# Kernel tuning notes

Measured on AMD Instinct MI355X. Metric: run time of the kernel, lower is better.

The kernel has to match this reference:

```python
import jax, jax.numpy as jnp
import numpy as np
import math

EPS = 1e-8
DIM, HEADS, K = 256, 8, 16
HD = DIM // HEADS
B, N, PDIM = 4, 4096, 3


def _layernorm(x, w, b, eps=1e-5):
    m = jnp.mean(x, axis=-1, keepdims=True)
    v = jnp.mean((x - m) ** 2, axis=-1, keepdims=True)
    return (x - m) * jax.lax.rsqrt(v + eps) * w + b


def setup_inputs() -> dict:
    key = jax.random.key(0)
    ks = jax.random.split(key, 16)
    s = 0.02
    d = {
        'x': jax.random.normal(ks[0], (B, N, DIM), jnp.float32),
        'positions': jax.random.uniform(ks[1], (B, N, PDIM), jnp.float32) * 0.5,  # inside unit ball
        'c': jnp.ones((1,), jnp.float32),
        'time_emb': jax.random.normal(ks[2], (B, DIM), jnp.float32),
        'Wq': jax.random.normal(ks[3], (DIM, DIM), jnp.float32) * s,
        'bq': jnp.zeros((DIM,), jnp.float32),
        'Wk': jax.random.normal(ks[4], (DIM, DIM), jnp.float32) * s,
        'bk': jnp.zeros((DIM,), jnp.float32),
        'Wv': jax.random.normal(ks[5], (DIM, DIM), jnp.float32) * s,
        'bv': jnp.zeros((DIM,), jnp.float32),
        'Wo': jax.random.normal(ks[6], (DIM, DIM), jnp.float32) * s,
        'bo': jnp.zeros((DIM,), jnp.float32),
        'W1': jax.random.normal(ks[7], (DIM, 4 * DIM), jnp.float32) * s,
        'b1': jnp.zeros((4 * DIM,), jnp.float32),
        'W2': jax.random.normal(ks[8], (4 * DIM, DIM), jnp.float32) * s,
        'b2': jnp.zeros((DIM,), jnp.float32),
        'ln1_w': jnp.ones((DIM,), jnp.float32),
        'ln1_b': jnp.zeros((DIM,), jnp.float32),
        'ln2_w': jnp.ones((DIM,), jnp.float32),
        'ln2_b': jnp.zeros((DIM,), jnp.float32),
        'log_tau': jnp.zeros((), jnp.float32),
    }
    return d


def _poincare_dist_matrix(pos, c):
    # pos: [B,N,P], c: scalar > 0. Returns [B,N,N] with d[b,i,j] = dist(pos[b,j], pos[b,i])
    sq = jnp.sum(pos ** 2, axis=-1)                      # [B,N]
    diff2 = (sq[:, :, None] + sq[:, None, :]
             - 2.0 * jnp.einsum('bip,bjp->bij', pos, pos))
    diff2 = jnp.maximum(diff2, 0.0)
    num = 2.0 * c * diff2
    den = (1.0 - c * sq[:, :, None]) * (1.0 - c * sq[:, None, :])
    arg = jnp.maximum(1.0 + num / (den + EPS), 1.0)
    return jnp.arccosh(arg) / jnp.sqrt(c)


def reference(x, positions, c, time_emb, Wq, bq, Wk, bk, Wv, bv, Wo, bo,
              W1, b1, W2, b2, ln1_w, ln1_b, ln2_w, ln2_b, log_tau):
    c_s = jnp.squeeze(c)
    x_res = x
    h = _layernorm(x, ln1_w, ln1_b) + time_emb[:, None, :]

    q = (h @ Wq + bq).reshape(B, N, HEADS, HD).transpose(0, 2, 1, 3)  # [B,H,N,hd]
    k = (h @ Wk + bk).reshape(B, N, HEADS, HD).transpose(0, 2, 1, 3)
    v = (h @ Wv + bv).reshape(B, N, HEADS, HD).transpose(0, 2, 1, 3)

    # pairwise hyperbolic distances + kNN (no_grad in original)
    dist = jax.lax.stop_gradient(_poincare_dist_matrix(positions, c_s))  # [B,N,N]
    neg_vals, idx = jax.lax.top_k(-dist, K)          # smallest-K distances
    attn_dists = -neg_vals                            # [B,N,K]

    # gather neighbor keys/values: out[b,h,n,j,d] = k[b,h,idx[b,n,j],d]
    idx_flat = idx.reshape(B, 1, N * K, 1)            # broadcast over heads, hd
    k_g = jnp.take_along_axis(k, idx_flat, axis=2).reshape(B, HEADS, N, K, HD)
    v_g = jnp.take_along_axis(v, idx_flat, axis=2).reshape(B, HEADS, N, K, HD)

    feat = jnp.einsum('bhnd,bhnkd->bhnk', q, k_g) / math.sqrt(HD)
    tau = jnp.exp(log_tau) + EPS
    scores = feat - attn_dists[:, None, :, :] / tau
    probs = jax.nn.softmax(scores, axis=-1)
    attn = jnp.einsum('bhnk,bhnkd->bhnd', probs, v_g)
    attn = attn.transpose(0, 2, 1, 3).reshape(B, N, DIM)

    x2 = x_res + attn @ Wo + bo
    ff = jax.nn.gelu(_layernorm(x2, ln2_w, ln2_b) @ W1 + b1, approximate=False) @ W2 + b2
    return x2 + ff
```

## Files before the change

kernel.cpp:

```cpp
#include <hip/hip_runtime.h>
#include <math.h>

namespace {

constexpr int kBatch = 4;
constexpr int kN = 4096;
constexpr int kDim = 256;
constexpr int kHeads = 8;
constexpr int kK = 16;
constexpr float kEps = 1e-8f;

using u16 = unsigned short;
typedef __attribute__((ext_vector_type(8))) short short8;
typedef __attribute__((ext_vector_type(8))) u16 u16x8;
typedef __attribute__((ext_vector_type(4))) float f32x4;

__device__ __forceinline__ float b2f(u16 u) {
  union { unsigned int i; float f; } x; x.i = ((unsigned int)u) << 16; return x.f;
}
__device__ __forceinline__ u16 f2b(float f) {
  union { float f; unsigned int i; } x; x.f = f;
  unsigned int r = x.i + 0x7fffu + ((x.i >> 16) & 1u);
  return (u16)(r >> 16);
}
__device__ __forceinline__ float gelu_exact(float x) {
  return 0.5f * x * (1.0f + erff(x * 0.70710678118654752f));
}
__device__ __forceinline__ void load_lds16(const u16* g, u16* l) {
  __builtin_amdgcn_global_load_lds(
      (const __attribute__((address_space(1))) unsigned int*)g,
      (__attribute__((address_space(3))) unsigned int*)l, 16, 0, 0);
}

template<bool ADD_TEMB>
__global__ __launch_bounds__(256) void ln_kernel(
    const float* __restrict__ x, const float* __restrict__ w,
    const float* __restrict__ bb, const float* __restrict__ temb,
    u16* __restrict__ out) {
  int gt = blockIdx.x * 256 + threadIdx.x;
  int row = gt >> 6;
  int lane = threadIdx.x & 63;
  const float4* xr = (const float4*)(x + (size_t)row * kDim);
  float4 v = xr[lane];
  float s = v.x + v.y + v.z + v.w;
  #pragma unroll
  for (int off = 32; off; off >>= 1) s += __shfl_xor(s, off);
  float mean = s * (1.0f / kDim);
  float dx = v.x - mean, dy = v.y - mean, dz = v.z - mean, dw = v.w - mean;
  float ss = dx * dx + dy * dy + dz * dz + dw * dw;
  #pragma unroll
  for (int off = 32; off; off >>= 1) ss += __shfl_xor(ss, off);
  float rstd = rsqrtf(ss * (1.0f / kDim) + 1e-5f);
  float4 wv = ((const float4*)w)[lane];
  float4 bv = ((const float4*)bb)[lane];
  float ox = dx * rstd * wv.x + bv.x;
  float oy = dy * rstd * wv.y + bv.y;
  float oz = dz * rstd * wv.z + bv.z;
  float ow = dw * rstd * wv.w + bv.w;
  if (ADD_TEMB) {
    int bi = row >> 12;
    float4 t = ((const float4*)(temb + (size_t)bi * kDim))[lane];
    ox += t.x; oy += t.y; oz += t.z; ow += t.w;
  }
  ushort4 ob;
  ob.x = f2b(ox); ob.y = f2b(oy); ob.z = f2b(oz); ob.w = f2b(ow);
  ((ushort4*)(out + (size_t)row * kDim))[lane] = ob;
}

__global__ __launch_bounds__(256) void wtrans_kernel(
    const float* __restrict__ Wq, const float* __restrict__ Wk,
    const float* __restrict__ Wv, const float* __restrict__ Wo,
    const float* __restrict__ W1, const float* __restrict__ W2,
    u16* __restrict__ Tq, u16* __restrict__ Tk,
    u16* __restrict__ Tv, u16* __restrict__ To,
    u16* __restrict__ T1, u16* __restrict__ T2) {
  __shared__ float t[32][33];
  int bx = blockIdx.x;
  int seg = bx >> 8, e = bx & 255;
  const float* W; u16* T; int Kin, Nin, kt, nt;
  if (seg == 0) {
    int which = e >> 6, tl = e & 63;
    W = which == 0 ? Wq : which == 1 ? Wk : which == 2 ? Wv : Wo;
    T = which == 0 ? Tq : which == 1 ? Tk : which == 2 ? Tv : To;
    Kin = 256; Nin = 256; kt = tl >> 3; nt = tl & 7;
  } else if (seg == 1) {
    W = W1; T = T1; Kin = 256; Nin = 1024; kt = e >> 5; nt = e & 31;
  } else {
    W = W2; T = T2; Kin = 1024; Nin = 256; kt = e >> 3; nt = e & 7;
  }
  int tx = threadIdx.x & 31, ty = threadIdx.x >> 5;
  #pragma unroll
  for (int rr = 0; rr < 4; ++rr) {
    int r = rr * 8 + ty;
    t[r][tx] = W[(size_t)(kt * 32 + r) * Nin + nt * 32 + tx];
  }
  __syncthreads();
  #pragma unroll
  for (int rr = 0; rr < 4; ++rr) {
    int r = rr * 8 + ty;
    T[(size_t)(nt * 32 + r) * Kin + kt * 32 + tx] = f2b(t[tx][r]);
  }
}

template<int EPI, int BN>
__device__ __forceinline__ void gemm_body(
    const u16* __restrict__ A, const u16* __restrict__ Bt,
    const float* __restrict__ bias, const float* __restrict__ R,
    float* __restrict__ Cf, u16* __restrict__ Cbf,
    int N, int K, int bx, int by) {
  constexpr int NI = BN / 32;
  __shared__ u16 Al[128 * 32];
  __shared__ u16 Bl[BN * 32];
  int tid = threadIdx.x;
  int wv = tid >> 6, ln = tid & 63;
  int wr = wv >> 1, wc = wv & 1;
  int lhi = ln >> 4, llo = ln & 15;
  int bm = bx * 128, bn = by * BN;

  f32x4 zero = {0.f, 0.f, 0.f, 0.f};
  f32x4 acc[4][NI];
  #pragma unroll
  for (int mi = 0; mi < 4; ++mi)
    #pragma unroll
    for (int ni = 0; ni < NI; ++ni) acc[mi][ni] = zero;

  for (int k0 = 0; k0 < K; k0 += 32) {
    if (k0) __syncthreads();
    #pragma unroll
    for (int i = 0; i < 2; ++i) {
      int f = i * 256 + tid;
      int r = f >> 2, kp = f & 3;
      load_lds16(A + (size_t)(bm + r) * K + k0 + kp * 8,
                 &Al[(i * 256 + wv * 64) * 8]);
    }
    #pragma unroll
    for (int i = 0; i < BN / 64; ++i) {
      int f = i * 256 + tid;
      int r = f >> 2, kp = f & 3;
      load_lds16(Bt + (size_t)(bn + r) * K + k0 + kp * 8,
                 &Bl[(i * 256 + wv * 64) * 8]);
    }
    __syncthreads();
    short8 af[4], bf[NI];
    #pragma unroll
    for (int mi = 0; mi < 4; ++mi)
      af[mi] = *(const short8*)&Al[(wr * 64 + mi * 16 + llo) * 32 + lhi * 8];
    #pragma unroll
    for (int ni = 0; ni < NI; ++ni)
      bf[ni] = *(const short8*)&Bl[(wc * (BN / 2) + ni * 16 + llo) * 32 + lhi * 8];
    #pragma unroll
    for (int mi = 0; mi < 4; ++mi)
      #pragma unroll
      for (int ni = 0; ni < NI; ++ni)
        acc[mi][ni] = __builtin_amdgcn_mfma_f32_16x16x32_bf16(
            af[mi], bf[ni], acc[mi][ni], 0, 0, 0);
  }

  #pragma unroll
  for (int mi = 0; mi < 4; ++mi) {
    #pragma unroll
    for (int r = 0; r < 4; ++r) {
      int row = bm + wr * 64 + mi * 16 + lhi * 4 + r;
      #pragma unroll
      for (int ni = 0; ni < NI; ++ni) {
        int col = bn + wc * (BN / 2) + ni * 16 + llo;
        float val = acc[mi][ni][r] + bias[col];
        if (EPI == 1) {
          val += R[(size_t)row * N + col];
          Cf[(size_t)row * N + col] = val;
        } else {
          if (EPI == 2) val = gelu_exact(val);
          Cbf[(size_t)row * N + col] = f2b(val);
        }
      }
    }
  }
}

template<int EPI, int BN>
__global__ __launch_bounds__(256) void gemm_kernel(
    const u16* __restrict__ A, const u16* __restrict__ Bt,
    const float* __restrict__ bias, const float* __restrict__ R,
    float* __restrict__ Cf, u16* __restrict__ Cbf, int N, int K) {
  gemm_body<EPI, BN>(A, Bt, bias, R, Cf, Cbf, N, K, blockIdx.x, blockIdx.y);
}

__global__ __launch_bounds__(256) void qkv_kernel(
    const u16* __restrict__ A,
    const u16* __restrict__ Bq, const u16* __restrict__ Bk, const u16* __restrict__ Bv,
    const float* __restrict__ bq, const float* __restrict__ bk, const float* __restrict__ bv,
    u16* __restrict__ q, u16* __restrict__ k, u16* __restrict__ v) {
  int sel = blockIdx.y >> 1;
  const u16* Bt = sel == 0 ? Bq : sel == 1 ? Bk : Bv;
  const float* bias = sel == 0 ? bq : sel == 1 ? bk : bv;
  u16* C = sel == 0 ? q : sel == 1 ? k : v;
  gemm_body<0, 128>(A, Bt, bias, nullptr, nullptr, C, 256, 256,
                    blockIdx.x, blockIdx.y & 1);
}

__global__ __launch_bounds__(1024, 4) void topk_kernel(
    const float* __restrict__ pos, const float* __restrict__ cptr,
    int* __restrict__ idx_out, float* __restrict__ dist_out) {
  __shared__ float4 ps[kN];
  int tid = threadIdx.x;
  int wave = tid >> 6, ln = tid & 63;
  int row = blockIdx.x * 16 + wave;
  int b = row >> 12;
  float c = cptr[0];
  const float* pb = pos + (size_t)b * kN * 3;
  for (int j = tid; j < kN; j += 1024) {
    float x = pb[j * 3 + 0], y = pb[j * 3 + 1], z = pb[j * 3 + 2];
    ps[j] = make_float4(x, y, z, c * (x * x + y * y + z * z));
  }
  __syncthreads();

  int i = row & (kN - 1);
  float4 pi = ps[i];
  float wi = pi.w, oi = 1.0f - wi;
  float sx = 2.0f * c * pi.x, sy = 2.0f * c * pi.y, sz = 2.0f * c * pi.z;

  auto numden = [&](int j, float& num, float& den) {
    float4 pj = ps[j];
    float tt = wi + pj.w;
    tt = fmaf(-sx, pj.x, tt);
    tt = fmaf(-sy, pj.y, tt);
    tt = fmaf(-sz, pj.z, tt);
    num = fmaxf(tt, 0.0f);
    den = fmaf(-oi, pj.w, oi);
  };
  auto packkey = [&](float num, float den, int j) -> unsigned {
    float r = num * __builtin_amdgcn_rcpf(den);
    union { float f; unsigned u; } cv; cv.f = r;
    return (cv.u & 0xFFFFF000u) | (unsigned)j;
  };
  auto inflate = [&](unsigned T) -> float {
    union { unsigned u; float f; } tv; tv.u = T & 0xFFFFF000u;
    return fmaf(tv.f, 0.001f, tv.f);
  };

  float n0, d0;
  numden(ln, n0, d0);
  unsigned lpk = packkey(n0, d0, ln);
  #pragma unroll
  for (int kk = 2; kk <= 64; kk <<= 1) {
    #pragma unroll
    for (int jj = kk >> 1; jj >= 1; jj >>= 1) {
      unsigned ov = (unsigned)__shfl_xor((int)lpk, jj);
      bool keepMin = (((ln & kk) == 0) == ((ln & jj) == 0));
      bool less = ov < lpk;
      if (keepMin ? less : !less) lpk = ov;
    }
  }
  float Tf = inflate((unsigned)__builtin_amdgcn_readlane((int)lpk, 15));

  auto processGroup = [&](float num, float den, int base) {
    unsigned long long m = __ballot(num < Tf * den);
    if (m) {
      unsigned cpk = packkey(num, den, base + ln);
      do {
        int src = __ffsll(m) - 1;
        m &= m - 1;
        unsigned npk = (unsigned)__builtin_amdgcn_readlane((int)cpk, src);
        unsigned pv = (unsigned)__builtin_amdgcn_update_dpp(
            0, (int)lpk, 0x111 , 0xF, 0xF, false);
        bool gt = lpk > npk;
        bool take = gt && ((ln == 0) || (pv <= npk));
        lpk = take ? npk : (gt ? pv : lpk);
      } while (m);
      Tf = inflate((unsigned)__builtin_amdgcn_readlane((int)lpk, 15));
    }
  };

  int t = 1;
  for (; t + 3 < 64; t += 4) {
    float a0, b0, a1, b1, a2, b2, a3, b3;
    numden(ln + (t + 0) * 64, a0, b0);
    numden(ln + (t + 1) * 64, a1, b1);
    numden(ln + (t + 2) * 64, a2, b2);
    numden(ln + (t + 3) * 64, a3, b3);
    processGroup(a0, b0, (t + 0) * 64);
    processGroup(a1, b1, (t + 1) * 64);
    processGroup(a2, b2, (t + 2) * 64);
    processGroup(a3, b3, (t + 3) * 64);
  }
  for (; t < 64; ++t) {
    float a0, b0;
    numden(ln + t * 64, a0, b0);
    processGroup(a0, b0, t * 64);
  }

  if (ln < kK) {
    int j = (int)(lpk & 0xFFFu);
    float4 pj = ps[j];
    float tt = wi + pj.w;
    tt = fmaf(-sx, pj.x, tt);
    tt = fmaf(-sy, pj.y, tt);
    tt = fmaf(-sz, pj.z, tt);
    float num = 2.0f * fmaxf(tt, 0.0f);
    float den = fmaf(-oi, pj.w, oi) + kEps;
    float arg = fmaxf(1.0f + num / den, 1.0f);
    float rs = 1.0f / sqrtf(c);
    idx_out[(size_t)row * kK + ln] = j;
    dist_out[(size_t)row * kK + ln] = acoshf(arg) * rs;
  }
}

__global__ __launch_bounds__(256) void attn_kernel(
    const u16* __restrict__ q, const u16* __restrict__ k,
    const u16* __restrict__ v, const int* __restrict__ nidx,
    const float* __restrict__ ndist, const float* __restrict__ log_tau,
    u16* __restrict__ out) {
  int t = blockIdx.x * 256 + threadIdx.x;
  int h = t & (kHeads - 1);
  int row = t >> 3;
  int b = row >> 12;
  float rtau = 1.0f / (expf(log_tau[0]) + kEps);
  const u16x8* qr = (const u16x8*)(q + (size_t)row * kDim + h * 32);
  float qf[32];
  #pragma unroll
  for (int cch = 0; cch < 4; ++cch) {
    u16x8 u = qr[cch];
    #pragma unroll
    for (int e = 0; e < 8; ++e) qf[cch * 8 + e] = b2f(u[e]);
  }

  int njs[kK];
  float sc[kK];
  const int* ir = nidx + (size_t)row * kK;
  const float* dr = ndist + (size_t)row * kK;
  float smax = -1e30f;
  #pragma unroll
  for (int j = 0; j < kK; ++j) {
    int nj = ir[j];
    njs[j] = nj;
    const u16x8* kr = (const u16x8*)(k + ((size_t)b * kN + nj) * kDim + h * 32);
    float dot = 0.0f;
    #pragma unroll
    for (int cch = 0; cch < 4; ++cch) {
      u16x8 u = kr[cch];
      #pragma unroll
      for (int e = 0; e < 8; ++e) dot = fmaf(qf[cch * 8 + e], b2f(u[e]), dot);
    }
    float s = dot * 0.17677669529663687f - dr[j] * rtau;
    sc[j] = s;
    smax = fmaxf(smax, s);
  }
  float sum = 0.0f;
  #pragma unroll
  for (int j = 0; j < kK; ++j) { sc[j] = expf(sc[j] - smax); sum += sc[j]; }
  float rsum = 1.0f / sum;
  float o[32];
  #pragma unroll
  for (int d = 0; d < 32; ++d) o[d] = 0.0f;
  #pragma unroll
  for (int j = 0; j < kK; ++j) {
    float p = sc[j] * rsum;
    const u16x8* vr = (const u16x8*)(v + ((size_t)b * kN + njs[j]) * kDim + h * 32);
    #pragma unroll
    for (int cch = 0; cch < 4; ++cch) {
      u16x8 u = vr[cch];
      #pragma unroll
      for (int e = 0; e < 8; ++e) o[cch * 8 + e] = fmaf(p, b2f(u[e]), o[cch * 8 + e]);
    }
  }
  u16x8* orow = (u16x8*)(out + (size_t)row * kDim + h * 32);
  #pragma unroll
  for (int cch = 0; cch < 4; ++cch) {
    u16x8 po;
    #pragma unroll
    for (int e = 0; e < 8; ++e) po[e] = f2b(o[cch * 8 + e]);
    orow[cch] = po;
  }
}

}

extern "C" void kernel_launch(void* const* d_in, const int* in_sizes, int n_in,
                              void* d_out, int out_size, void* d_ws, size_t ws_size,
                              hipStream_t stream) {
  const float* x    = (const float*)d_in[0];
  const float* pos  = (const float*)d_in[1];
  const float* c    = (const float*)d_in[2];
  const float* temb = (const float*)d_in[3];
  const float* Wq   = (const float*)d_in[4];
  const float* bq   = (const float*)d_in[5];
  const float* Wk   = (const float*)d_in[6];
  const float* bk   = (const float*)d_in[7];
  const float* Wv   = (const float*)d_in[8];
  const float* bv   = (const float*)d_in[9];
  const float* Wo   = (const float*)d_in[10];
  const float* bo   = (const float*)d_in[11];
  const float* W1   = (const float*)d_in[12];
  const float* b1   = (const float*)d_in[13];
  const float* W2   = (const float*)d_in[14];
  const float* b2   = (const float*)d_in[15];
  const float* ln1w = (const float*)d_in[16];
  const float* ln1b = (const float*)d_in[17];
  const float* ln2w = (const float*)d_in[18];
  const float* ln2b = (const float*)d_in[19];
  const float* ltau = (const float*)d_in[20];

  const size_t MB = 1ull << 20;
  char* w = (char*)d_ws;
  u16*   h_bf  = (u16*)(w + 0 * MB);
  u16*   qb    = (u16*)(w + 8 * MB);
  u16*   kb    = (u16*)(w + 16 * MB);
  u16*   vb    = (u16*)(w + 24 * MB);
  u16*   attnb = (u16*)(w + 32 * MB);
  float* x2    = (float*)(w + 40 * MB);
  u16*   g_bf  = (u16*)(w + 56 * MB);
  u16*   wq_t  = (u16*)(w + 88 * MB);
  u16*   wk_t  = wq_t + 65536;
  u16*   wv_t  = wq_t + 2 * 65536;
  u16*   wo_t  = wq_t + 3 * 65536;
  u16*   w1_t  = (u16*)(w + 89 * MB);
  u16*   w2_t  = (u16*)(w + 89 * MB + 512 * 1024);
  int*   kidx  = (int*)(w + 90 * MB);
  float* kdst  = (float*)(w + 91 * MB);
  u16*   tln   = h_bf;

  hipLaunchKernelGGL(wtrans_kernel, dim3(768), dim3(256), 0, stream,
                     Wq, Wk, Wv, Wo, W1, W2, wq_t, wk_t, wv_t, wo_t, w1_t, w2_t);
  hipLaunchKernelGGL((ln_kernel<true>), dim3(4096), dim3(256), 0, stream,
                     x, ln1w, ln1b, temb, h_bf);
  hipLaunchKernelGGL(topk_kernel, dim3(1024), dim3(1024), 0, stream,
                     pos, c, kidx, kdst);
  hipLaunchKernelGGL(qkv_kernel, dim3(128, 6), dim3(256), 0, stream,
                     h_bf, wq_t, wk_t, wv_t, bq, bk, bv, qb, kb, vb);
  hipLaunchKernelGGL(attn_kernel, dim3(512), dim3(256), 0, stream,
                     qb, kb, vb, kidx, kdst, ltau, attnb);
  hipLaunchKernelGGL((gemm_kernel<1, 64>), dim3(128, 4), dim3(256), 0, stream,
                     attnb, wo_t, bo, x, x2, (u16*)nullptr, 256, 256);
  hipLaunchKernelGGL((ln_kernel<false>), dim3(4096), dim3(256), 0, stream,
                     x2, ln2w, ln2b, nullptr, tln);
  hipLaunchKernelGGL((gemm_kernel<2, 128>), dim3(128, 8), dim3(256), 0, stream,
                     tln, w1_t, b1, nullptr, (float*)nullptr, g_bf, 1024, 256);
  hipLaunchKernelGGL((gemm_kernel<1, 64>), dim3(128, 4), dim3(256), 0, stream,
                     g_bf, w2_t, b2, x2, (float*)d_out, (u16*)nullptr, 256, 1024);
}
```

Measured before the change: 179.5 us.

## Restructure GEMMs to stage whole B panels in swizzled LDS and stream A from registers

All GEMM kernels (QKV, output projection, FFN1, FFN2) are rewritten so that a 64-column B panel is staged into LDS in large K chunks with an XOR swizzle against bank conflicts. A operands are read straight from global memory into registers instead of through LDS, and there are far fewer barriers per K step. The grids now use BN=64 tiles, which doubles the block count for QKV and FFN1. The intent is to cut synchronization and LDS traffic. In exchange, the non-coalesced direct global A loads may go uncached and the larger LDS footprint may lower occupancy.

```diff
diff --git a/kernel.cpp b/kernel.cpp
--- a/kernel.cpp
+++ b/kernel.cpp
@@ -102,58 +102,61 @@
   }
 }
 
-template<int EPI, int BN>
-__device__ __forceinline__ void gemm_body(
+template<int EPI, int KTOT, int KCHUNK>
+__global__ __launch_bounds__(256) void gemm2_kernel(
     const u16* __restrict__ A, const u16* __restrict__ Bt,
     const float* __restrict__ bias, const float* __restrict__ R,
-    float* __restrict__ Cf, u16* __restrict__ Cbf,
-    int N, int K, int bx, int by) {
-  constexpr int NI = BN / 32;
-  __shared__ u16 Al[128 * 32];
-  __shared__ u16 Bl[BN * 32];
+    float* __restrict__ Cf, u16* __restrict__ Cbf, int N) {
+  __shared__ u16 Bl[64 * KCHUNK];
+  constexpr int OCT = KCHUNK / 8;
   int tid = threadIdx.x;
   int wv = tid >> 6, ln = tid & 63;
   int wr = wv >> 1, wc = wv & 1;
   int lhi = ln >> 4, llo = ln & 15;
-  int bm = bx * 128, bn = by * BN;
+  int bm = blockIdx.x * 128, bn = blockIdx.y * 64;
 
   f32x4 zero = {0.f, 0.f, 0.f, 0.f};
-  f32x4 acc[4][NI];
+  f32x4 acc[4][2];
   #pragma unroll
   for (int mi = 0; mi < 4; ++mi)
     #pragma unroll
-    for (int ni = 0; ni < NI; ++ni) acc[mi][ni] = zero;
-
-  for (int k0 = 0; k0 < K; k0 += 32) {
-    if (k0) __syncthreads();
-    #pragma unroll
-    for (int i = 0; i < 2; ++i) {
+    for (int ni = 0; ni < 2; ++ni) acc[mi][ni] = zero;
+
+  const u16* Arow[4];
+  #pragma unroll
+  for (int mi = 0; mi < 4; ++mi)
+    Arow[mi] = A + (size_t)(bm + wr * 64 + mi * 16 + llo) * KTOT + lhi * 8;
+
+  for (int kc = 0; kc < KTOT; kc += KCHUNK) {
+    if (kc) __syncthreads();
+    constexpr int NL = 64 * KCHUNK / (8 * 256);
+    #pragma unroll
+    for (int i = 0; i < NL; ++i) {
       int f = i * 256 + tid;
-      int r = f >> 2, kp = f & 3;
-      load_lds16(A + (size_t)(bm + r) * K + k0 + kp * 8,
-                 &Al[(i * 256 + wv * 64) * 8]);
-    }
-    #pragma unroll
-    for (int i = 0; i < BN / 64; ++i) {
-      int f = i * 256 + tid;
-      int r = f >> 2, kp = f & 3;
-      load_lds16(Bt + (size_t)(bn + r) * K + k0 + kp * 8,
+      int r = f / OCT, o = f % OCT;
+      load_lds16(Bt + (size_t)(bn + r) * KTOT + kc + ((o ^ (r & 7)) << 3),
                  &Bl[(i * 256 + wv * 64) * 8]);
     }
     __syncthreads();
-    short8 af[4], bf[NI];
-    #pragma unroll
-    for (int mi = 0; mi < 4; ++mi)
-      af[mi] = *(const short8*)&Al[(wr * 64 + mi * 16 + llo) * 32 + lhi * 8];
-    #pragma unroll
-    for (int ni = 0; ni < NI; ++ni)
-      bf[ni] = *(const short8*)&Bl[(wc * (BN / 2) + ni * 16 + llo) * 32 + lhi * 8];
-    #pragma unroll
-    for (int mi = 0; mi < 4; ++mi)
-      #pragma unroll
-      for (int ni = 0; ni < NI; ++ni)
-        acc[mi][ni] = __builtin_amdgcn_mfma_f32_16x16x32_bf16(
-            af[mi], bf[ni], acc[mi][ni], 0, 0, 0);
+    #pragma unroll
+    for (int k0 = 0; k0 < KCHUNK; k0 += 32) {
+      short8 af[4], bf[2];
+      #pragma unroll
+      for (int mi = 0; mi < 4; ++mi)
+        af[mi] = *(const short8*)(Arow[mi] + kc + k0);
+      #pragma unroll
+      for (int ni = 0; ni < 2; ++ni) {
+        int brow = wc * 32 + ni * 16 + llo;
+        int oct = ((k0 >> 3) + lhi) ^ (llo & 7);
+        bf[ni] = *(const short8*)&Bl[brow * KCHUNK + oct * 8];
+      }
+      #pragma unroll
+      for (int mi = 0; mi < 4; ++mi)
+        #pragma unroll
+        for (int ni = 0; ni < 2; ++ni)
+          acc[mi][ni] = __builtin_amdgcn_mfma_f32_16x16x32_bf16(
+              af[mi], bf[ni], acc[mi][ni], 0, 0, 0);
+    }
   }
 
   #pragma unroll
@@ -162,8 +165,8 @@
     for (int r = 0; r < 4; ++r) {
       int row = bm + wr * 64 + mi * 16 + lhi * 4 + r;
       #pragma unroll
-      for (int ni = 0; ni < NI; ++ni) {
-        int col = bn + wc * (BN / 2) + ni * 16 + llo;
+      for (int ni = 0; ni < 2; ++ni) {
+        int col = bn + wc * 32 + ni * 16 + llo;
         float val = acc[mi][ni][r] + bias[col];
         if (EPI == 1) {
           val += R[(size_t)row * N + col];
@@ -177,25 +180,72 @@
   }
 }
 
-template<int EPI, int BN>
-__global__ __launch_bounds__(256) void gemm_kernel(
-    const u16* __restrict__ A, const u16* __restrict__ Bt,
-    const float* __restrict__ bias, const float* __restrict__ R,
-    float* __restrict__ Cf, u16* __restrict__ Cbf, int N, int K) {
-  gemm_body<EPI, BN>(A, Bt, bias, R, Cf, Cbf, N, K, blockIdx.x, blockIdx.y);
-}
-
-__global__ __launch_bounds__(256) void qkv_kernel(
+__global__ __launch_bounds__(256) void qkv2_kernel(
     const u16* __restrict__ A,
     const u16* __restrict__ Bq, const u16* __restrict__ Bk, const u16* __restrict__ Bv,
     const float* __restrict__ bq, const float* __restrict__ bk, const float* __restrict__ bv,
     u16* __restrict__ q, u16* __restrict__ k, u16* __restrict__ v) {
-  int sel = blockIdx.y >> 1;
+  __shared__ u16 Bl[64 * 256];
+  int sel = blockIdx.y >> 2, by = blockIdx.y & 3;
   const u16* Bt = sel == 0 ? Bq : sel == 1 ? Bk : Bv;
   const float* bias = sel == 0 ? bq : sel == 1 ? bk : bv;
   u16* C = sel == 0 ? q : sel == 1 ? k : v;
-  gemm_body<0, 128>(A, Bt, bias, nullptr, nullptr, C, 256, 256,
-                    blockIdx.x, blockIdx.y & 1);
+
+  int tid = threadIdx.x;
+  int wv = tid >> 6, ln = tid & 63;
+  int wr = wv >> 1, wc = wv & 1;
+  int lhi = ln >> 4, llo = ln & 15;
+  int bm = blockIdx.x * 128, bn = by * 64;
+
+  f32x4 zero = {0.f, 0.f, 0.f, 0.f};
+  f32x4 acc[4][2];
+  #pragma unroll
+  for (int mi = 0; mi < 4; ++mi)
+    #pragma unroll
+    for (int ni = 0; ni < 2; ++ni) acc[mi][ni] = zero;
+
+  #pragma unroll
+  for (int i = 0; i < 8; ++i) {
+    int f = i * 256 + tid;
+    int r = f >> 5, o = f & 31;
+    load_lds16(Bt + (size_t)(bn + r) * 256 + ((o ^ (r & 7)) << 3),
+               &Bl[(i * 256 + wv * 64) * 8]);
+  }
+  __syncthreads();
+  const u16* Arow[4];
+  #pragma unroll
+  for (int mi = 0; mi < 4; ++mi)
+    Arow[mi] = A + (size_t)(bm + wr * 64 + mi * 16 + llo) * 256 + lhi * 8;
+  #pragma unroll
+  for (int k0 = 0; k0 < 256; k0 += 32) {
+    short8 af[4], bf[2];
+    #pragma unroll
+    for (int mi = 0; mi < 4; ++mi) af[mi] = *(const short8*)(Arow[mi] + k0);
+    #pragma unroll
+    for (int ni = 0; ni < 2; ++ni) {
+      int brow = wc * 32 + ni * 16 + llo;
+      int oct = ((k0 >> 3) + lhi) ^ (llo & 7);
+      bf[ni] = *(const short8*)&Bl[brow * 256 + oct * 8];
+    }
+    #pragma unroll
+    for (int mi = 0; mi < 4; ++mi)
+      #pragma unroll
+      for (int ni = 0; ni < 2; ++ni)
+        acc[mi][ni] = __builtin_amdgcn_mfma_f32_16x16x32_bf16(
+            af[mi], bf[ni], acc[mi][ni], 0, 0, 0);
+  }
+  #pragma unroll
+  for (int mi = 0; mi < 4; ++mi) {
+    #pragma unroll
+    for (int r = 0; r < 4; ++r) {
+      int row = bm + wr * 64 + mi * 16 + lhi * 4 + r;
+      #pragma unroll
+      for (int ni = 0; ni < 2; ++ni) {
+        int col = bn + wc * 32 + ni * 16 + llo;
+        C[(size_t)row * 256 + col] = f2b(acc[mi][ni][r] + bias[col]);
+      }
+    }
+  }
 }
 
 __global__ __launch_bounds__(1024, 4) void topk_kernel(
@@ -425,16 +475,16 @@
                      x, ln1w, ln1b, temb, h_bf);
   hipLaunchKernelGGL(topk_kernel, dim3(1024), dim3(1024), 0, stream,
                      pos, c, kidx, kdst);
-  hipLaunchKernelGGL(qkv_kernel, dim3(128, 6), dim3(256), 0, stream,
+  hipLaunchKernelGGL(qkv2_kernel, dim3(128, 12), dim3(256), 0, stream,
                      h_bf, wq_t, wk_t, wv_t, bq, bk, bv, qb, kb, vb);
   hipLaunchKernelGGL(attn_kernel, dim3(512), dim3(256), 0, stream,
                      qb, kb, vb, kidx, kdst, ltau, attnb);
-  hipLaunchKernelGGL((gemm_kernel<1, 64>), dim3(128, 4), dim3(256), 0, stream,
-                     attnb, wo_t, bo, x, x2, (u16*)nullptr, 256, 256);
+  hipLaunchKernelGGL((gemm2_kernel<1, 256, 256>), dim3(128, 4), dim3(256), 0, stream,
+                     attnb, wo_t, bo, x, x2, (u16*)nullptr, 256);
   hipLaunchKernelGGL((ln_kernel<false>), dim3(4096), dim3(256), 0, stream,
                      x2, ln2w, ln2b, nullptr, tln);
-  hipLaunchKernelGGL((gemm_kernel<2, 128>), dim3(128, 8), dim3(256), 0, stream,
-                     tln, w1_t, b1, nullptr, (float*)nullptr, g_bf, 1024, 256);
-  hipLaunchKernelGGL((gemm_kernel<1, 64>), dim3(128, 4), dim3(256), 0, stream,
-                     g_bf, w2_t, b2, x2, (float*)d_out, (u16*)nullptr, 256, 1024);
-}
+  hipLaunchKernelGGL((gemm2_kernel<2, 256, 256>), dim3(128, 16), dim3(256), 0, stream,
+                     tln, w1_t, b1, nullptr, (float*)nullptr, g_bf, 1024);
+  hipLaunchKernelGGL((gemm2_kernel<1, 1024, 256>), dim3(128, 4), dim3(256), 0, stream,
+                     g_bf, w2_t, b2, x2, (float*)d_out, (u16*)nullptr, 256);
+}
```

Result: slower. 222.9 us (+24.2%).

## Double GEMM K-tile to 64 and XOR-swizzle LDS layout to avoid bank conflicts

Applied to the files above, without the earlier changes.

Raises the bf16 MFMA GEMM's shared-memory K-tile from 32 to 64, halving the number of global-to-LDS load rounds and barriers per output tile. It also XOR-swizzles the 16-byte octets within each LDS row, keyed on the row index, so that the MFMA fragment reads from LDS spread across banks instead of colliding. The cost is double the LDS per block, which may lower occupancy, plus extra index arithmetic.

```diff
diff --git a/kernel.cpp b/kernel.cpp
--- a/kernel.cpp
+++ b/kernel.cpp
@@ -109,8 +109,9 @@
     float* __restrict__ Cf, u16* __restrict__ Cbf,
     int N, int K, int bx, int by) {
   constexpr int NI = BN / 32;
-  __shared__ u16 Al[128 * 32];
-  __shared__ u16 Bl[BN * 32];
+  constexpr int BK = 64;
+  __shared__ u16 Al[128 * BK];
+  __shared__ u16 Bl[BN * BK];
   int tid = threadIdx.x;
   int wv = tid >> 6, ln = tid & 63;
   int wr = wv >> 1, wc = wv & 1;
@@ -124,36 +125,45 @@
     #pragma unroll
     for (int ni = 0; ni < NI; ++ni) acc[mi][ni] = zero;
 
-  for (int k0 = 0; k0 < K; k0 += 32) {
+  for (int k0 = 0; k0 < K; k0 += BK) {
     if (k0) __syncthreads();
     #pragma unroll
-    for (int i = 0; i < 2; ++i) {
+    for (int i = 0; i < 128 * BK / (8 * 256); ++i) {
       int f = i * 256 + tid;
-      int r = f >> 2, kp = f & 3;
-      load_lds16(A + (size_t)(bm + r) * K + k0 + kp * 8,
+      int r = f >> 3, o = f & 7;
+      load_lds16(A + (size_t)(bm + r) * K + k0 + ((o ^ (r & 7)) << 3),
                  &Al[(i * 256 + wv * 64) * 8]);
     }
     #pragma unroll
-    for (int i = 0; i < BN / 64; ++i) {
+    for (int i = 0; i < BN * BK / (8 * 256); ++i) {
       int f = i * 256 + tid;
-      int r = f >> 2, kp = f & 3;
-      load_lds16(Bt + (size_t)(bn + r) * K + k0 + kp * 8,
+      int r = f >> 3, o = f & 7;
+      load_lds16(Bt + (size_t)(bn + r) * K + k0 + ((o ^ (r & 7)) << 3),
                  &Bl[(i * 256 + wv * 64) * 8]);
     }
     __syncthreads();
-    short8 af[4], bf[NI];
-    #pragma unroll
-    for (int mi = 0; mi < 4; ++mi)
-      af[mi] = *(const short8*)&Al[(wr * 64 + mi * 16 + llo) * 32 + lhi * 8];
-    #pragma unroll
-    for (int ni = 0; ni < NI; ++ni)
-      bf[ni] = *(const short8*)&Bl[(wc * (BN / 2) + ni * 16 + llo) * 32 + lhi * 8];
-    #pragma unroll
-    for (int mi = 0; mi < 4; ++mi)
-      #pragma unroll
-      for (int ni = 0; ni < NI; ++ni)
-        acc[mi][ni] = __builtin_amdgcn_mfma_f32_16x16x32_bf16(
-            af[mi], bf[ni], acc[mi][ni], 0, 0, 0);
+    #pragma unroll
+    for (int ks = 0; ks < BK; ks += 32) {
+      short8 af[4], bf[NI];
+      #pragma unroll
+      for (int mi = 0; mi < 4; ++mi) {
+        int row = wr * 64 + mi * 16 + llo;
+        int oct = ((ks >> 3) + lhi) ^ (llo & 7);
+        af[mi] = *(const short8*)&Al[row * BK + oct * 8];
+      }
+      #pragma unroll
+      for (int ni = 0; ni < NI; ++ni) {
+        int row = wc * (BN / 2) + ni * 16 + llo;
+        int oct = ((ks >> 3) + lhi) ^ (llo & 7);
+        bf[ni] = *(const short8*)&Bl[row * BK + oct * 8];
+      }
+      #pragma unroll
+      for (int mi = 0; mi < 4; ++mi)
+        #pragma unroll
+        for (int ni = 0; ni < NI; ++ni)
+          acc[mi][ni] = __builtin_amdgcn_mfma_f32_16x16x32_bf16(
+              af[mi], bf[ni], acc[mi][ni], 0, 0, 0);
+    }
   }
 
   #pragma unroll
```

New measurement: 179.9 us. About the same (+0.2%).
